# Kernel optimization log

Measured on AMD Instinct MI355X. Metric: run time of the kernel, lower is better.

The kernel has to match this reference:

```python
import jax, jax.numpy as jnp
import numpy as np
from jax import lax

NUM_MARKETS = 32
WINDOW = 16
T = 1048576


def setup_inputs() -> dict:
    key = jax.random.key(0)
    k1, k2, k3, k4 = jax.random.split(key, 4)
    std = float(np.sqrt(WINDOW))  # matches nn.init.normal_(.., 0, sqrt(window_size))
    x = jax.random.normal(k1, (1, NUM_MARKETS, T), dtype=jnp.float32)
    start_pos = -jnp.ones((NUM_MARKETS, 1), dtype=jnp.float32)  # default start_pos = -1
    conv_w = jax.random.normal(k2, (NUM_MARKETS, NUM_MARKETS, WINDOW), dtype=jnp.float32) * std
    conv_b = jax.random.normal(k3, (NUM_MARKETS,), dtype=jnp.float32) * 0.05
    pos_weight = jax.random.normal(k4, (NUM_MARKETS, 1), dtype=jnp.float32) * std
    return {"x": x, "start_pos": start_pos, "conv_w": conv_w, "conv_b": conv_b, "pos_weight": pos_weight}


def reference(x, start_pos, conv_w, conv_b, pos_weight):
    # Conv1d, valid padding: [1, N, T] -> [1, N, L], L = T - WINDOW + 1
    y = lax.conv_general_dilated(
        x, conv_w, window_strides=(1,), padding="VALID",
        dimension_numbers=("NCH", "OIH", "NCH"),
    ) + conv_b[None, :, None]
    seq = y[0].T  # [L, N] time-major for the scan
    pw = pos_weight[:, 0]  # [N]

    def step(pos, xt):
        a = jnp.tanh(pos * pw + xt)  # [N]
        return jnp.sign(a), a

    _, outs = lax.scan(step, start_pos[:, 0], seq)  # outs: [L, N]
    positions = jnp.concatenate([start_pos, outs.T], axis=1)  # [N, L+1]
    return positions[None]  # [1, N, L+1]
```

## Files before the change

kernel.cpp:

```cpp
#include <hip/hip_runtime.h>
#include <stdint.h>

#define T_LEN    1048576
#define TY_LEN   1048561
#define OUT_W    1048562
#define NM       32
#define WIN      16
#define NBLK     4096
#define CBT      256
#define TPB      256
#define XS_W     272
#define NF4      68
#define ID8      0xE4u
#define FLG_AGG  0x40000000u
#define FLG_INC  0x80000000u

__device__ inline float sgnf(float a){
    return (a > 0.0f) ? 1.0f : ((a < 0.0f) ? -1.0f : 0.0f);
}

__device__ inline uint32_t comp2(uint32_t f, uint32_t g){
    uint32_t r = 0;
#pragma unroll
    for (int k = 0; k < 4; ++k) {
        const uint32_t s = (g >> (2 * k)) & 3u;
        r |= ((f >> (2 * s)) & 3u) << (2 * k);
    }
    return r;
}

__global__ void wtrans_kernel(const float* __restrict__ w, float* __restrict__ wT2){
    const int idx = blockIdx.x * 256 + threadIdx.x;
    if (idx >= NM * NM * WIN) return;
    const int o = idx / (NM * WIN);
    const int r = idx - o * (NM * WIN);
    const int i = r / WIN;
    const int h = r - i * WIN;
    wT2[(((h * 4) + (o >> 3)) * NM + i) * 8 + (o & 7)] = w[idx];
}

__global__ __launch_bounds__(256, 4) void conv_kernel(
    const float* __restrict__ x, const float* __restrict__ wT2,
    const float* __restrict__ b, const float* __restrict__ sp,
    const float* __restrict__ pwv, float* __restrict__ out,
    uint32_t* __restrict__ agg)
{
    __shared__ float xs[NM * XS_W];
    __shared__ uint32_t maps8[256];
    const int bid  = blockIdx.x;
    const int base = bid * TPB;
    for (int idx = threadIdx.x; idx < NM * NF4; idx += CBT) {
        const int i = idx / NF4;
        const int q = idx - i * NF4;
        const int t0 = base + q * 4;
        float4 v;
        if (t0 + 3 < T_LEN) {
            v = *reinterpret_cast<const float4*>(x + (size_t)i * T_LEN + t0);
        } else {
            v.x = (t0 + 0 < T_LEN) ? x[(size_t)i * T_LEN + t0 + 0] : 0.0f;
            v.y = (t0 + 1 < T_LEN) ? x[(size_t)i * T_LEN + t0 + 1] : 0.0f;
            v.z = (t0 + 2 < T_LEN) ? x[(size_t)i * T_LEN + t0 + 2] : 0.0f;
            v.w = (t0 + 3 < T_LEN) ? x[(size_t)i * T_LEN + t0 + 3] : 0.0f;
        }
        *reinterpret_cast<float4*>(&xs[i * XS_W + q * 4]) = v;
    }
    __syncthreads();
    const int lane = threadIdx.x & 63;
    const int og   = __builtin_amdgcn_readfirstlane(threadIdx.x >> 6);
    float acc[8][4];
#pragma unroll
    for (int oi = 0; oi < 8; ++oi)
#pragma unroll
        for (int tt = 0; tt < 4; ++tt) acc[oi][tt] = 0.0f;
#pragma unroll 1
    for (int h = 0; h < WIN; ++h) {
        const float* wp = wT2 + (size_t)(h * 4 + og) * (NM * 8);
#pragma unroll 1
        for (int c = 0; c < 4; ++c) {
            float xv[8][4];
#pragma unroll
            for (int i2 = 0; i2 < 8; ++i2) {
                const int i = c * 8 + i2;
#pragma unroll
                for (int tt = 0; tt < 4; ++tt)
                    xv[i2][tt] = xs[i * XS_W + lane + 64 * tt + h];
            }
#pragma unroll
            for (int i2 = 0; i2 < 8; ++i2) {
                const float* wr = wp + (c * 8 + i2) * 8;
#pragma unroll
                for (int oi = 0; oi < 8; ++oi) {
                    const float wv = wr[oi];
#pragma unroll
                    for (int tt = 0; tt < 4; ++tt)
                        acc[oi][tt] = fmaf(wv, xv[i2][tt], acc[oi][tt]);
                }
            }
        }
    }
    __syncthreads();
#pragma unroll
    for (int oi = 0; oi < 8; ++oi) {
        const int o = og * 8 + oi;
        const float bv = b[o];
#pragma unroll
        for (int tt = 0; tt < 4; ++tt) {
            const int sub = (lane >> 5) + 2 * tt;
            xs[(o * 8 + sub) * 33 + (lane & 31)] = acc[oi][tt] + bv;
        }
    }
    __syncthreads();
    const int sm = threadIdx.x >> 3;
    const int ss = threadIdx.x & 7;
    const float pws = pwv[sm];
    const float spv = sp[sm];
    int st = TY_LEN - base - ss * 32;
    st = st < 0 ? 0 : (st > 32 ? 32 : st);
    {
        float q0 = -1.0f, q1 = 0.0f, q2 = 1.0f, q3 = spv;
        const float* yr = &xs[(sm * 8 + ss) * 33];
        for (int j = 0; j < st; ++j) {
            const float hv = yr[j];
            q0 = sgnf(fmaf(q0, pws, hv));
            q1 = sgnf(fmaf(q1, pws, hv));
            q2 = sgnf(fmaf(q2, pws, hv));
            q3 = sgnf(fmaf(q3, pws, hv));
        }
        const uint32_t e0 = (uint32_t)((int)q0 + 1);
        const uint32_t e1 = (uint32_t)((int)q1 + 1);
        const uint32_t e2 = (uint32_t)((int)q2 + 1);
        const uint32_t e3 = (st == 0) ? 3u : (uint32_t)((int)q3 + 1);
        maps8[threadIdx.x] = e0 | (e1 << 2) | (e2 << 4) | (e3 << 6);
    }
    __syncthreads();
    uint32_t* ar = agg + (size_t)sm * NBLK;
    if (ss == 0) {
        uint32_t seg = ID8;
#pragma unroll
        for (int s2 = 0; s2 < 8; ++s2) seg = comp2(maps8[sm * 8 + s2], seg);
        __hip_atomic_store(&ar[bid], FLG_AGG | seg,
                           __ATOMIC_RELAXED, __HIP_MEMORY_SCOPE_AGENT);
    }
    uint32_t prefix = ID8;
    {
        int wstart = bid - 8;
        bool done = (bid == 0);
        while (!done) {
            const int idx = wstart + ss;
            uint32_t w;
            if (idx < 0) {
                w = FLG_INC | ID8;
            } else {
                w = __hip_atomic_load(&ar[idx], __ATOMIC_RELAXED,
                                      __HIP_MEMORY_SCOPE_AGENT);
                while (!(w & 0xC0000000u)) {
                    __builtin_amdgcn_s_sleep(1);
                    w = __hip_atomic_load(&ar[idx], __ATOMIC_RELAXED,
                                          __HIP_MEMORY_SCOPE_AGENT);
                }
            }
            uint32_t cur = prefix;
            bool stop = false;
#pragma unroll
            for (int k = 7; k >= 0; --k) {
                const uint32_t wk = __shfl(w, (threadIdx.x & 56) | k, 64);
                if (!stop) {
                    cur = comp2(cur, wk & 0xFFu);
                    if (wk & FLG_INC) stop = true;
                }
            }
            prefix = cur;
            done = stop;
            wstart -= 8;
        }
    }
    if (ss == 0) {
        uint32_t Aown = ID8;
#pragma unroll
        for (int s2 = 0; s2 < 8; ++s2) Aown = comp2(maps8[sm * 8 + s2], Aown);
        __hip_atomic_store(&ar[bid], FLG_INC | comp2(Aown, prefix),
                           __ATOMIC_RELAXED, __HIP_MEMORY_SCOPE_AGENT);
    }
    {
        uint32_t s = (prefix >> 6) & 3u;
        for (int k = 0; k < ss; ++k) s = (maps8[sm * 8 + k] >> (2 * s)) & 3u;
        float p = (s == 3u) ? spv : ((float)(int)s - 1.0f);
        float* yr = &xs[(sm * 8 + ss) * 33];
        for (int j = 0; j < st; ++j) {
            const float a = fmaf(p, pws, yr[j]);
            yr[j] = tanhf(a);
            p = sgnf(a);
        }
    }
    __syncthreads();
#pragma unroll
    for (int oi = 0; oi < 8; ++oi) {
        const int o = og * 8 + oi;
        float* orow = out + (size_t)o * OUT_W + 1 + base + lane;
#pragma unroll
        for (int tt = 0; tt < 4; ++tt) {
            const int t = base + lane + 64 * tt;
            const int sub = (lane >> 5) + 2 * tt;
            if (t < TY_LEN) orow[64 * tt] = xs[(o * 8 + sub) * 33 + (lane & 31)];
        }
    }
    if (bid == 0 && threadIdx.x < NM)
        out[(size_t)threadIdx.x * OUT_W] = sp[threadIdx.x];
}

extern "C" void kernel_launch(void* const* d_in, const int* in_sizes, int n_in,
                              void* d_out, int out_size, void* d_ws, size_t ws_size,
                              hipStream_t stream)
{
    const float* x   = (const float*)d_in[0];
    const float* spv = (const float*)d_in[1];
    const float* w   = (const float*)d_in[2];
    const float* b   = (const float*)d_in[3];
    const float* pw  = (const float*)d_in[4];
    float* out = (float*)d_out;

    uint8_t* ws = (uint8_t*)d_ws;
    float*    wT2 = (float*)ws;
    uint32_t* agg = (uint32_t*)(ws + 65536);

    hipMemsetAsync(agg, 0, (size_t)NM * NBLK * 4, stream);
    wtrans_kernel<<<64, 256, 0, stream>>>(w, wT2);
    conv_kernel<<<NBLK, CBT, 0, stream>>>(x, wT2, b, spv, pw, out, agg);
}
```

Measured before the change: 425.6 us.

## Stage inputs and weights into LDS via async global_load_lds, fold memset into prep kernel

The x tile is now loaded straight into shared memory with global_load_lds for every block except the last. Per-tap weights are double-buffered in LDS and read as float4 broadcasts instead of per-element scalar global loads. The separate agg memset is merged into the weight-transpose kernel, which saves one launch. The larger LDS footprint makes launch bounds drop from 4 to 3 blocks per CU, and each tap iteration now adds a block-wide barrier and vmcnt wait, so lower occupancy could offset the gains.

```diff
diff --git a/kernel.cpp b/kernel.cpp
--- a/kernel.cpp
+++ b/kernel.cpp
@@ -29,44 +29,59 @@
     return r;
 }
 
-__global__ void wtrans_kernel(const float* __restrict__ w, float* __restrict__ wT2){
+__device__ inline void gload16(const void* g, void* l){
+    __builtin_amdgcn_global_load_lds(
+        (const __attribute__((address_space(1))) unsigned int*)g,
+        (__attribute__((address_space(3))) unsigned int*)l, 16, 0, 0);
+}
+
+__global__ void wtrans_kernel(const float* __restrict__ w, float* __restrict__ wT2,
+                              uint32_t* __restrict__ agg){
     const int idx = blockIdx.x * 256 + threadIdx.x;
-    if (idx >= NM * NM * WIN) return;
-    const int o = idx / (NM * WIN);
-    const int r = idx - o * (NM * WIN);
-    const int i = r / WIN;
-    const int h = r - i * WIN;
-    wT2[(((h * 4) + (o >> 3)) * NM + i) * 8 + (o & 7)] = w[idx];
-}
-
-__global__ __launch_bounds__(256, 4) void conv_kernel(
+    if (idx < NM * NM * WIN) {
+        const int o = idx / (NM * WIN);
+        const int r = idx - o * (NM * WIN);
+        const int i = r / WIN;
+        const int h = r - i * WIN;
+        wT2[(((h * 4) + (o >> 3)) * NM + i) * 8 + (o & 7)] = w[idx];
+    }
+    for (int j = idx; j < NM * NBLK; j += 64 * 256) agg[j] = 0;
+}
+
+__global__ __launch_bounds__(256, 3) void conv_kernel(
     const float* __restrict__ x, const float* __restrict__ wT2,
     const float* __restrict__ b, const float* __restrict__ sp,
     const float* __restrict__ pwv, float* __restrict__ out,
     uint32_t* __restrict__ agg)
 {
     __shared__ float xs[NM * XS_W];
+    __shared__ float wlds[2][1024];
     __shared__ uint32_t maps8[256];
     const int bid  = blockIdx.x;
     const int base = bid * TPB;
-    for (int idx = threadIdx.x; idx < NM * NF4; idx += CBT) {
-        const int i = idx / NF4;
-        const int q = idx - i * NF4;
-        const int t0 = base + q * 4;
-        float4 v;
-        if (t0 + 3 < T_LEN) {
-            v = *reinterpret_cast<const float4*>(x + (size_t)i * T_LEN + t0);
-        } else {
+    const int tid  = threadIdx.x;
+    if (bid != NBLK - 1) {
+        for (int idx = tid; idx < NM * NF4; idx += CBT) {
+            const int i = idx / NF4;
+            const int q = idx - i * NF4;
+            gload16(x + (size_t)i * T_LEN + base + q * 4, &xs[idx * 4]);
+        }
+    } else {
+        for (int idx = tid; idx < NM * NF4; idx += CBT) {
+            const int i = idx / NF4;
+            const int q = idx - i * NF4;
+            const int t0 = base + q * 4;
+            float4 v;
             v.x = (t0 + 0 < T_LEN) ? x[(size_t)i * T_LEN + t0 + 0] : 0.0f;
             v.y = (t0 + 1 < T_LEN) ? x[(size_t)i * T_LEN + t0 + 1] : 0.0f;
             v.z = (t0 + 2 < T_LEN) ? x[(size_t)i * T_LEN + t0 + 2] : 0.0f;
             v.w = (t0 + 3 < T_LEN) ? x[(size_t)i * T_LEN + t0 + 3] : 0.0f;
-        }
-        *reinterpret_cast<float4*>(&xs[i * XS_W + q * 4]) = v;
-    }
-    __syncthreads();
-    const int lane = threadIdx.x & 63;
-    const int og   = __builtin_amdgcn_readfirstlane(threadIdx.x >> 6);
+            *reinterpret_cast<float4*>(&xs[i * XS_W + q * 4]) = v;
+        }
+    }
+    gload16(wT2 + tid * 4, &wlds[0][tid * 4]);
+    const int lane = tid & 63;
+    const int og   = __builtin_amdgcn_readfirstlane(tid >> 6);
     float acc[8][4];
 #pragma unroll
     for (int oi = 0; oi < 8; ++oi)
@@ -74,7 +89,12 @@
         for (int tt = 0; tt < 4; ++tt) acc[oi][tt] = 0.0f;
 #pragma unroll 1
     for (int h = 0; h < WIN; ++h) {
-        const float* wp = wT2 + (size_t)(h * 4 + og) * (NM * 8);
+        asm volatile("s_waitcnt vmcnt(0)" ::: "memory");
+        __syncthreads();
+        if (h + 1 < WIN)
+            gload16(wT2 + (size_t)(h + 1) * 1024 + tid * 4,
+                    &wlds[(h + 1) & 1][tid * 4]);
+        const float* wb = &wlds[h & 1][og * 256];
 #pragma unroll 1
         for (int c = 0; c < 4; ++c) {
             float xv[8][4];
@@ -87,13 +107,19 @@
             }
 #pragma unroll
             for (int i2 = 0; i2 < 8; ++i2) {
-                const float* wr = wp + (c * 8 + i2) * 8;
-#pragma unroll
-                for (int oi = 0; oi < 8; ++oi) {
-                    const float wv = wr[oi];
-#pragma unroll
-                    for (int tt = 0; tt < 4; ++tt)
-                        acc[oi][tt] = fmaf(wv, xv[i2][tt], acc[oi][tt]);
+                const float* wr = wb + (c * 8 + i2) * 8;
+                const float4 w0 = *reinterpret_cast<const float4*>(wr);
+                const float4 w1 = *reinterpret_cast<const float4*>(wr + 4);
+#pragma unroll
+                for (int tt = 0; tt < 4; ++tt) {
+                    acc[0][tt] = fmaf(w0.x, xv[i2][tt], acc[0][tt]);
+                    acc[1][tt] = fmaf(w0.y, xv[i2][tt], acc[1][tt]);
+                    acc[2][tt] = fmaf(w0.z, xv[i2][tt], acc[2][tt]);
+                    acc[3][tt] = fmaf(w0.w, xv[i2][tt], acc[3][tt]);
+                    acc[4][tt] = fmaf(w1.x, xv[i2][tt], acc[4][tt]);
+                    acc[5][tt] = fmaf(w1.y, xv[i2][tt], acc[5][tt]);
+                    acc[6][tt] = fmaf(w1.z, xv[i2][tt], acc[6][tt]);
+                    acc[7][tt] = fmaf(w1.w, xv[i2][tt], acc[7][tt]);
                 }
             }
         }
@@ -110,8 +136,8 @@
         }
     }
     __syncthreads();
-    const int sm = threadIdx.x >> 3;
-    const int ss = threadIdx.x & 7;
+    const int sm = tid >> 3;
+    const int ss = tid & 7;
     const float pws = pwv[sm];
     const float spv = sp[sm];
     int st = TY_LEN - base - ss * 32;
@@ -130,7 +156,7 @@
         const uint32_t e1 = (uint32_t)((int)q1 + 1);
         const uint32_t e2 = (uint32_t)((int)q2 + 1);
         const uint32_t e3 = (st == 0) ? 3u : (uint32_t)((int)q3 + 1);
-        maps8[threadIdx.x] = e0 | (e1 << 2) | (e2 << 4) | (e3 << 6);
+        maps8[tid] = e0 | (e1 << 2) | (e2 << 4) | (e3 << 6);
     }
     __syncthreads();
     uint32_t* ar = agg + (size_t)sm * NBLK;
@@ -163,7 +189,7 @@
             bool stop = false;
 #pragma unroll
             for (int k = 7; k >= 0; --k) {
-                const uint32_t wk = __shfl(w, (threadIdx.x & 56) | k, 64);
+                const uint32_t wk = __shfl(w, (tid & 56) | k, 64);
                 if (!stop) {
                     cur = comp2(cur, wk & 0xFFu);
                     if (wk & FLG_INC) stop = true;
@@ -204,8 +230,8 @@
             if (t < TY_LEN) orow[64 * tt] = xs[(o * 8 + sub) * 33 + (lane & 31)];
         }
     }
-    if (bid == 0 && threadIdx.x < NM)
-        out[(size_t)threadIdx.x * OUT_W] = sp[threadIdx.x];
+    if (bid == 0 && tid < NM)
+        out[(size_t)tid * OUT_W] = sp[tid];
 }
 
 extern "C" void kernel_launch(void* const* d_in, const int* in_sizes, int n_in,
@@ -223,7 +249,6 @@
     float*    wT2 = (float*)ws;
     uint32_t* agg = (uint32_t*)(ws + 65536);
 
-    hipMemsetAsync(agg, 0, (size_t)NM * NBLK * 4, stream);
-    wtrans_kernel<<<64, 256, 0, stream>>>(w, wT2);
+    wtrans_kernel<<<64, 256, 0, stream>>>(w, wT2, agg);
     conv_kernel<<<NBLK, CBT, 0, stream>>>(x, wT2, b, spv, pw, out, agg);
 }
```

Measured after the change: 477.6 us. 1.12x slower.
